# Kernel optimization log

Hardware: AMD Instinct MI355X
Metric: run time of the kernel (lower is better)

## Reference

```python
import jax, jax.numpy as jnp
import numpy as np

R_FRAC = 0.5  # r_token


def setup_inputs() -> dict:
    key = jax.random.key(0)
    B, T, C = 64, 577, 1024
    hidden_states = jax.random.normal(key, (B, T, C), dtype=jnp.float32)
    return {"hidden_states": hidden_states}


def _match_indices(x, r):
    # Bipartite soft matching (class_token=True, distill_token=False).
    metric = x / jnp.linalg.norm(x, axis=-1, keepdims=True)
    a, b = metric[:, ::2, :], metric[:, 1::2, :]  # [B, Ta, C], [B, Tb, C]
    scores = jnp.einsum('bic,bjc->bij', a, b)     # [B, Ta, Tb]
    scores = scores.at[:, 0, :].set(-jnp.inf)     # protect CLS token (even index 0)
    node_max = scores.max(axis=-1)                # best sim of each src to any dst
    node_idx = scores.argmax(axis=-1)             # matched dst for each src
    edge_idx = jnp.argsort(-node_max, axis=-1)    # descending by similarity
    unm_idx = jnp.sort(edge_idx[:, r:], axis=-1)  # unmerged src (sorted: keeps CLS first)
    src_idx = edge_idx[:, :r]                     # src tokens to merge
    dst_idx = jnp.take_along_axis(node_idx, src_idx, axis=-1)
    return unm_idx, src_idx, dst_idx


def _merge_sum(v, unm_idx, src_idx, dst_idx):
    # Gather unmerged + scatter-add merged src into dst, then concat.
    src, dst = v[:, ::2, :], v[:, 1::2, :]
    unm = jnp.take_along_axis(src, unm_idx[..., None], axis=1)
    srcg = jnp.take_along_axis(src, src_idx[..., None], axis=1)
    dst = jax.vmap(lambda d, i, s: d.at[i].add(s))(dst, dst_idx, srcg)
    return jnp.concatenate([unm, dst], axis=1)


def reference(hidden_states):
    x = hidden_states
    B, T, C = x.shape
    protected = 1  # class token
    r = min(int(R_FRAC * T), (T - protected) // 2)  # 288 for T=577
    unm_idx, src_idx, dst_idx = _match_indices(x, r)
    # merge_wavg with size=None -> size = ones
    size = jnp.ones((B, T, 1), dtype=x.dtype)
    xm = _merge_sum(x * size, unm_idx, src_idx, dst_idx)
    sm = _merge_sum(size, unm_idx, src_idx, dst_idx)
    return xm / sm  # [B, T - r, C]
```

## Files before the change

kernel.cpp:

```cpp
#include <hip/hip_runtime.h>
#include <math.h>


#define B_   64
#define T_   577
#define C_   1024
#define NA   289
#define NB   288
#define EPS_MARGIN 0.04f

#define RPAD 384
#define EXTRA_CAP 12

typedef __bf16 bf16x8 __attribute__((ext_vector_type(8)));
typedef float  floatx4 __attribute__((ext_vector_type(4)));
typedef unsigned long long u64;

#define ECNT_OFF   0
#define GRPWIN_OFF 98304
#define EXTRA_OFF  (GRPWIN_OFF + 1179648)
#define DST_OFF    (EXTRA_OFF + 2359296)

__device__ __forceinline__ u64 shfl_xor_u64(u64 v, int msk) {
  unsigned int lo = (unsigned int)v, hi = (unsigned int)(v >> 32);
  lo = __shfl_xor(lo, msk, 64);
  hi = __shfl_xor(hi, msk, 64);
  return ((u64)hi << 32) | (u64)lo;
}
__device__ __forceinline__ double shfl_xor_f64(double v, int msk) {
  u64 u = __double_as_longlong(v);
  return __longlong_as_double((long long)shfl_xor_u64(u, msk));
}

__device__ __forceinline__ unsigned int fkey(float s) {
  unsigned int fb = __float_as_uint(s);
  return (fb & 0x80000000u) ? ~fb : (fb | 0x80000000u);
}
__device__ __forceinline__ float keyf(unsigned int k) {
  return (k & 0x80000000u) ? __uint_as_float(k ^ 0x80000000u) : __uint_as_float(~k);
}
__device__ __forceinline__ u64 packsc(float s, int col) {
  return ((u64)fkey(s) << 32) | (u64)(0xFFFFFFFFu - (unsigned int)col);
}
__device__ __forceinline__ int pcol(u64 p) {
  return (int)(0xFFFFFFFFu - (unsigned int)(p & 0xFFFFFFFFull));
}
__device__ __forceinline__ float pscore(u64 p) { return keyf((unsigned int)(p >> 32)); }

__device__ __forceinline__ unsigned int pk_bf16_trunc(unsigned int e1, unsigned int e0) {
  return __builtin_amdgcn_perm(e1, e0, 0x07060302u);
}

__device__ __forceinline__ void load16f(const float* x, size_t off, float* v) {
  const float4* p = (const float4*)(x + off);
  float4 a = p[0], b = p[1], c = p[2], d = p[3];
  v[0]=a.x; v[1]=a.y; v[2]=a.z; v[3]=a.w;
  v[4]=b.x; v[5]=b.y; v[6]=b.z; v[7]=b.w;
  v[8]=c.x; v[9]=c.y; v[10]=c.z; v[11]=c.w;
  v[12]=d.x; v[13]=d.y; v[14]=d.z; v[15]=d.w;
}

__global__ __launch_bounds__(256, 2) void k_scores(const float* __restrict__ x,
                                                   u64* __restrict__ grpwin,
                                                   unsigned int* __restrict__ ecnt,
                                                   u64* __restrict__ extras) {
  __shared__ unsigned char smem[24576];
  __shared__ float sumsq[96];
  int tid = threadIdx.x;
  int b  = blockIdx.x;
  int rt = blockIdx.y;
  int ct = blockIdx.z;
  int wv = tid >> 6, lane = tid & 63;
  int m = lane & 15, q = lane >> 4;
  int sw = m & 7;

  if (tid < 96) sumsq[tid] = 0.f;

  floatx4 acc[3][3];
#pragma unroll
  for (int ii = 0; ii < 3; ++ii)
#pragma unroll
    for (int jj = 0; jj < 3; ++jj) acc[ii][jj] = (floatx4){0,0,0,0};

  const int ib = (wv >> 1) * 3;
  const int jb = (wv & 1) * 3;

  for (int kc = 0; kc < 16; ++kc) {
    int k0 = kc * 64;
    __syncthreads();
    for (int v = tid; v < 1536; v += 256) {
      int isB  = v >= 768;
      int w    = isB ? v - 768 : v;
      int row  = w >> 3, slot = w & 7;
      int gk   = slot ^ (row & 7);
      int tok;
      if (isB) tok = 2 * (ct * 96 + row) + 1;
      else { tok = 2 * (rt * 96 + row); if (tok > 576) tok = 576; }
      const uint4* src = (const uint4*)(x + (size_t)(b * T_ + tok) * C_ + k0 + gk * 8);
      uint4 lo = src[0], hi = src[1];
      uint4 o;
      o.x = pk_bf16_trunc(lo.y, lo.x);
      o.y = pk_bf16_trunc(lo.w, lo.z);
      o.z = pk_bf16_trunc(hi.y, hi.x);
      o.w = pk_bf16_trunc(hi.w, hi.z);
      *(uint4*)(smem + (isB ? 12288 : 0) + row * 128 + slot * 16) = o;
      if (isB) {
        float f0 = __uint_as_float(lo.x), f1 = __uint_as_float(lo.y);
        float f2 = __uint_as_float(lo.z), f3 = __uint_as_float(lo.w);
        float f4 = __uint_as_float(hi.x), f5 = __uint_as_float(hi.y);
        float f6 = __uint_as_float(hi.z), f7 = __uint_as_float(hi.w);
        float ss = f0*f0 + f1*f1 + f2*f2 + f3*f3 + f4*f4 + f5*f5 + f6*f6 + f7*f7;
        atomicAdd(&sumsq[row], ss);
      }
    }
    __syncthreads();
#pragma unroll
    for (int s = 0; s < 2; ++s) {
      int slot = (s * 4 + q) ^ sw;
      bf16x8 af[3], bf[3];
#pragma unroll
      for (int ii = 0; ii < 3; ++ii)
        af[ii] = *(const bf16x8*)(smem + ((ib + ii) * 16 + m) * 128 + slot * 16);
#pragma unroll
      for (int jj = 0; jj < 3; ++jj)
        bf[jj] = *(const bf16x8*)(smem + 12288 + ((jb + jj) * 16 + m) * 128 + slot * 16);
#pragma unroll
      for (int ii = 0; ii < 3; ++ii)
#pragma unroll
        for (int jj = 0; jj < 3; ++jj)
          acc[ii][jj] = __builtin_amdgcn_mfma_f32_16x16x32_bf16(af[ii], bf[jj], acc[ii][jj], 0,0,0);
    }
  }

  float rn[3];
#pragma unroll
  for (int jj = 0; jj < 3; ++jj) rn[jj] = rsqrtf(sumsq[(jb + jj) * 16 + m]);

  int g = ct * 2 + (wv & 1);
#pragma unroll
  for (int ii = 0; ii < 3; ++ii) {
#pragma unroll
    for (int r = 0; r < 4; ++r) {
      u64 pj[3];
#pragma unroll
      for (int jj = 0; jj < 3; ++jj) {
        float s = acc[ii][jj][r] * rn[jj];
        pj[jj] = packsc(s, ct * 96 + (jb + jj) * 16 + m);
      }
      u64 pk = pj[0];
      if (pj[1] > pk) pk = pj[1];
      if (pj[2] > pk) pk = pj[2];
#pragma unroll
      for (int d = 1; d < 16; d <<= 1) {
        u64 o = shfl_xor_u64(pk, d);
        if (o > pk) pk = o;
      }
      int grow = rt * 96 + (ib + ii) * 16 + q * 4 + r;
      float thr = pscore(pk) - EPS_MARGIN;
      size_t rbase = (size_t)b * RPAD + grow;
#pragma unroll
      for (int jj = 0; jj < 3; ++jj) {
        if (pj[jj] != pk && pscore(pj[jj]) >= thr) {
          unsigned int idx = atomicAdd(&ecnt[rbase], 1u);
          if (idx < EXTRA_CAP) extras[rbase * EXTRA_CAP + idx] = pj[jj];
        }
      }
      if (m == 0) grpwin[rbase * 6 + g] = pk;
    }
  }
}

__global__ __launch_bounds__(256) void k_recheck(const float* __restrict__ x,
                                                 const u64* __restrict__ grpwin,
                                                 const unsigned int* __restrict__ ecnt,
                                                 const u64* __restrict__ extras,
                                                 int* __restrict__ dst) {
  int wid = threadIdx.x >> 6, lane = threadIdx.x & 63;
  int gw = blockIdx.x * 4 + wid;
  int b = gw / NB, i = gw - b * NB + 1;
  size_t rbase = (size_t)b * RPAD + i;

  u64 v = (lane < 6) ? grpwin[rbase * 6 + lane] : 0ull;
#pragma unroll
  for (int d = 1; d < 8; d <<= 1) {
    u64 o = shfl_xor_u64(v, d);
    if (o > v) v = o;
  }
  v = shfl_xor_u64(v, 0) , v = v;
  {
    unsigned int lo = (unsigned int)v, hi = (unsigned int)(v >> 32);
    lo = __shfl(lo, 0, 64); hi = __shfl(hi, 0, 64);
    v = ((u64)hi << 32) | lo;
  }
  float thr = pscore(v) - EPS_MARGIN;

  u64 cand[14]; int nc = 0;
#pragma unroll
  for (int t = 0; t < 6; ++t) {
    u64 w = grpwin[rbase * 6 + t];
    if (pscore(w) >= thr && nc < 14) cand[nc++] = w;
  }
  unsigned int ec = ecnt[rbase]; if (ec > EXTRA_CAP) ec = EXTRA_CAP;
  for (unsigned int t = 0; t < ec; ++t) {
    u64 w = extras[rbase * EXTRA_CAP + t];
    if (pscore(w) >= thr && nc < 14) cand[nc++] = w;
  }

  int best;
  if (nc <= 1) {
    best = pcol(v);
  } else {
    float av[16];
    load16f(x, (size_t)(b * T_ + 2 * i) * C_ + lane * 16, av);
    double bs = -1e300; int bc = 1 << 30;
    for (int c = 0; c < nc; ++c) {
      int col = pcol(cand[c]);
      float bv[16];
      load16f(x, (size_t)(b * T_ + 2 * col + 1) * C_ + lane * 16, bv);
      double dot = 0.0, nsq = 0.0;
#pragma unroll
      for (int t = 0; t < 16; ++t) {
        dot += (double)av[t] * (double)bv[t];
        nsq += (double)bv[t] * (double)bv[t];
      }
#pragma unroll
      for (int d = 32; d >= 1; d >>= 1) {
        dot += shfl_xor_f64(dot, d);
        nsq += shfl_xor_f64(nsq, d);
      }
      double s = dot / sqrt(nsq);
      if (s > bs || (s == bs && col < bc)) { bs = s; bc = col; }
    }
    best = bc;
  }
  if (lane == 0) dst[b * NA + i] = best;
}

__global__ __launch_bounds__(256) void k_merge(const float* __restrict__ x,
                                               const int* __restrict__ dst,
                                               float* __restrict__ out) {
  __shared__ int dstv[NA];
  __shared__ unsigned short lists[4][292];
  __shared__ int cnts[4];
  int b = blockIdx.y, tid = threadIdx.x;
  int orow_base = blockIdx.x * 4;

  for (int i = tid; i < NA; i += 256) dstv[i] = (i >= 1) ? dst[b * NA + i] : -1;
  if (tid < 4) cnts[tid] = 0;
  __syncthreads();

  for (int i = 1 + tid; i <= 288; i += 256) {
    int d = dstv[i];
#pragma unroll
    for (int w4 = 0; w4 < 4; ++w4) {
      int orow_w = orow_base + w4;
      if (orow_w >= 1 && orow_w < NA && d == orow_w - 1) {
        int idx = atomicAdd(&cnts[w4], 1);
        lists[w4][idx] = (unsigned short)i;
      }
    }
  }
  __syncthreads();

  int wv = tid >> 6, lane = tid & 63;
  int orow = orow_base + wv;
  if (orow >= NA) return;

  const size_t xb = (size_t)b * T_ * C_;
  int c0 = lane * 16;
  float acc[16];
  float inv = 1.0f;

  if (orow == 0) {
    load16f(x, xb + c0, acc);
  } else {
    int j = orow - 1;
    load16f(x, xb + (size_t)(2 * j + 1) * C_ + c0, acc);
    int cnt = cnts[wv];
    for (int e = 0; e < cnt; ++e) {
      int i = lists[wv][e];
      float tv[16];
      load16f(x, xb + (size_t)(2 * i) * C_ + c0, tv);
#pragma unroll
      for (int t = 0; t < 16; ++t) acc[t] += tv[t];
    }
    inv = 1.0f / (float)(cnt + 1);
  }

  float4* op = (float4*)(out + ((size_t)b * NA + orow) * C_ + c0);
  op[0] = make_float4(acc[0]*inv,  acc[1]*inv,  acc[2]*inv,  acc[3]*inv);
  op[1] = make_float4(acc[4]*inv,  acc[5]*inv,  acc[6]*inv,  acc[7]*inv);
  op[2] = make_float4(acc[8]*inv,  acc[9]*inv,  acc[10]*inv, acc[11]*inv);
  op[3] = make_float4(acc[12]*inv, acc[13]*inv, acc[14]*inv, acc[15]*inv);
}

extern "C" void kernel_launch(void* const* d_in, const int* in_sizes, int n_in,
                              void* d_out, int out_size, void* d_ws, size_t ws_size,
                              hipStream_t stream) {
  const float* x = (const float*)d_in[0];
  float* out     = (float*)d_out;
  char* ws = (char*)d_ws;
  unsigned int* ecnt = (unsigned int*)(ws + ECNT_OFF);
  u64* grpwin        = (u64*)(ws + GRPWIN_OFF);
  u64* extras        = (u64*)(ws + EXTRA_OFF);
  int* dst           = (int*)(ws + DST_OFF);

  hipMemsetAsync(ecnt, 0, (size_t)B_ * RPAD * sizeof(unsigned int), stream);
  k_scores <<<dim3(B_, 4, 3), 256, 0, stream>>>(x, grpwin, ecnt, extras);
  k_recheck<<<B_ * NB / 4, 256, 0, stream>>>(x, grpwin, ecnt, extras, dst);
  k_merge  <<<dim3((NA + 3) / 4, B_), 256, 0, stream>>>(x, dst, out);
}
```

Measured before the change: 341.5 us.

## Double-buffer LDS tiles and prefetch next K chunk in k_scores

Converts the k_scores main loop to a double-buffered LDS pipeline. Global loads for chunk kc+1 are issued into registers before the MFMA work on chunk kc, then converted to bf16 and stored into the other buffer, so each iteration needs one barrier instead of two. Per-thread partial sums of squares are kept in registers and written to shared memory with a single atomic each at the end, instead of one shared atomic per chunk. This doubles LDS use (about 48KB per block) and adds registers for the prefetch, which may hurt occupancy with launch_bounds(256,2).

New measurement: 309.1 us. 9.5% less time.

```diff
diff --git a/kernel.cpp b/kernel.cpp
--- a/kernel.cpp
+++ b/kernel.cpp
@@ -64,7 +64,7 @@
                                                    u64* __restrict__ grpwin,
                                                    unsigned int* __restrict__ ecnt,
                                                    u64* __restrict__ extras) {
-  __shared__ unsigned char smem[24576];
+  __shared__ unsigned char smem[2][24576];
   __shared__ float sumsq[96];
   int tid = threadIdx.x;
   int b  = blockIdx.x;
@@ -76,6 +76,49 @@
 
   if (tid < 96) sumsq[tid] = 0.f;
 
+  const float* eptr[6];
+  int eoff[6];
+#pragma unroll
+  for (int e = 0; e < 6; ++e) {
+    int v = tid + 256 * e;
+    int isB = v >= 768;
+    int w = isB ? v - 768 : v;
+    int row = w >> 3, slot = w & 7;
+    int gk = slot ^ (row & 7);
+    int tok;
+    if (isB) tok = 2 * (ct * 96 + row) + 1;
+    else { tok = 2 * (rt * 96 + row); if (tok > 576) tok = 576; }
+    eptr[e] = x + (size_t)(b * T_ + tok) * C_ + gk * 8;
+    eoff[e] = (isB ? 12288 : 0) + row * 128 + slot * 16;
+  }
+
+  float ssp[3] = {0.f, 0.f, 0.f};
+  uint4 L[6][2];
+
+#pragma unroll
+  for (int e = 0; e < 6; ++e) {
+    const uint4* p = (const uint4*)(eptr[e]);
+    L[e][0] = p[0]; L[e][1] = p[1];
+  }
+#pragma unroll
+  for (int e = 0; e < 6; ++e) {
+    uint4 lo = L[e][0], hi = L[e][1];
+    uint4 o;
+    o.x = pk_bf16_trunc(lo.y, lo.x);
+    o.y = pk_bf16_trunc(lo.w, lo.z);
+    o.z = pk_bf16_trunc(hi.y, hi.x);
+    o.w = pk_bf16_trunc(hi.w, hi.z);
+    *(uint4*)(smem[0] + eoff[e]) = o;
+    if (e >= 3) {
+      float f0 = __uint_as_float(lo.x), f1 = __uint_as_float(lo.y);
+      float f2 = __uint_as_float(lo.z), f3 = __uint_as_float(lo.w);
+      float f4 = __uint_as_float(hi.x), f5 = __uint_as_float(hi.y);
+      float f6 = __uint_as_float(hi.z), f7 = __uint_as_float(hi.w);
+      ssp[e-3] += f0*f0 + f1*f1 + f2*f2 + f3*f3 + f4*f4 + f5*f5 + f6*f6 + f7*f7;
+    }
+  }
+  __syncthreads();
+
   floatx4 acc[3][3];
 #pragma unroll
   for (int ii = 0; ii < 3; ++ii)
@@ -86,51 +129,59 @@
   const int jb = (wv & 1) * 3;
 
   for (int kc = 0; kc < 16; ++kc) {
-    int k0 = kc * 64;
-    __syncthreads();
-    for (int v = tid; v < 1536; v += 256) {
-      int isB  = v >= 768;
-      int w    = isB ? v - 768 : v;
-      int row  = w >> 3, slot = w & 7;
-      int gk   = slot ^ (row & 7);
-      int tok;
-      if (isB) tok = 2 * (ct * 96 + row) + 1;
-      else { tok = 2 * (rt * 96 + row); if (tok > 576) tok = 576; }
-      const uint4* src = (const uint4*)(x + (size_t)(b * T_ + tok) * C_ + k0 + gk * 8);
-      uint4 lo = src[0], hi = src[1];
-      uint4 o;
-      o.x = pk_bf16_trunc(lo.y, lo.x);
-      o.y = pk_bf16_trunc(lo.w, lo.z);
-      o.z = pk_bf16_trunc(hi.y, hi.x);
-      o.w = pk_bf16_trunc(hi.w, hi.z);
-      *(uint4*)(smem + (isB ? 12288 : 0) + row * 128 + slot * 16) = o;
-      if (isB) {
-        float f0 = __uint_as_float(lo.x), f1 = __uint_as_float(lo.y);
-        float f2 = __uint_as_float(lo.z), f3 = __uint_as_float(lo.w);
-        float f4 = __uint_as_float(hi.x), f5 = __uint_as_float(hi.y);
-        float f6 = __uint_as_float(hi.z), f7 = __uint_as_float(hi.w);
-        float ss = f0*f0 + f1*f1 + f2*f2 + f3*f3 + f4*f4 + f5*f5 + f6*f6 + f7*f7;
-        atomicAdd(&sumsq[row], ss);
-      }
-    }
-    __syncthreads();
+    const unsigned char* buf = smem[kc & 1];
+    unsigned char* nbuf = smem[(kc + 1) & 1];
+    if (kc < 15) {
+#pragma unroll
+      for (int e = 0; e < 6; ++e) {
+        const uint4* p = (const uint4*)(eptr[e] + (kc + 1) * 64);
+        L[e][0] = p[0]; L[e][1] = p[1];
+      }
+    }
 #pragma unroll
     for (int s = 0; s < 2; ++s) {
       int slot = (s * 4 + q) ^ sw;
       bf16x8 af[3], bf[3];
 #pragma unroll
       for (int ii = 0; ii < 3; ++ii)
-        af[ii] = *(const bf16x8*)(smem + ((ib + ii) * 16 + m) * 128 + slot * 16);
+        af[ii] = *(const bf16x8*)(buf + ((ib + ii) * 16 + m) * 128 + slot * 16);
 #pragma unroll
       for (int jj = 0; jj < 3; ++jj)
-        bf[jj] = *(const bf16x8*)(smem + 12288 + ((jb + jj) * 16 + m) * 128 + slot * 16);
+        bf[jj] = *(const bf16x8*)(buf + 12288 + ((jb + jj) * 16 + m) * 128 + slot * 16);
 #pragma unroll
       for (int ii = 0; ii < 3; ++ii)
 #pragma unroll
         for (int jj = 0; jj < 3; ++jj)
           acc[ii][jj] = __builtin_amdgcn_mfma_f32_16x16x32_bf16(af[ii], bf[jj], acc[ii][jj], 0,0,0);
     }
-  }
+    if (kc < 15) {
+#pragma unroll
+      for (int e = 0; e < 6; ++e) {
+        uint4 lo = L[e][0], hi = L[e][1];
+        uint4 o;
+        o.x = pk_bf16_trunc(lo.y, lo.x);
+        o.y = pk_bf16_trunc(lo.w, lo.z);
+        o.z = pk_bf16_trunc(hi.y, hi.x);
+        o.w = pk_bf16_trunc(hi.w, hi.z);
+        *(uint4*)(nbuf + eoff[e]) = o;
+        if (e >= 3) {
+          float f0 = __uint_as_float(lo.x), f1 = __uint_as_float(lo.y);
+          float f2 = __uint_as_float(lo.z), f3 = __uint_as_float(lo.w);
+          float f4 = __uint_as_float(hi.x), f5 = __uint_as_float(hi.y);
+          float f6 = __uint_as_float(hi.z), f7 = __uint_as_float(hi.w);
+          ssp[e-3] += f0*f0 + f1*f1 + f2*f2 + f3*f3 + f4*f4 + f5*f5 + f6*f6 + f7*f7;
+        }
+      }
+    }
+    __syncthreads();
+  }
+
+#pragma unroll
+  for (int e = 3; e < 6; ++e) {
+    int w = tid + 256 * e - 768;
+    atomicAdd(&sumsq[w >> 3], ssp[e-3]);
+  }
+  __syncthreads();
 
   float rn[3];
 #pragma unroll
@@ -186,7 +237,6 @@
     u64 o = shfl_xor_u64(v, d);
     if (o > v) v = o;
   }
-  v = shfl_xor_u64(v, 0) , v = v;
   {
     unsigned int lo = (unsigned int)v, hi = (unsigned int)(v >> 32);
     lo = __shfl(lo, 0, 64); hi = __shfl(hi, 0, 64);
```
